# Kernel tuning notes

Measured on AMD Instinct MI355X. Metric: run time of the kernel, lower is better.

Reference implementation:

```python
import jax, jax.numpy as jnp
import numpy as np

B = 16384
D_VIS, D_LANG, D_STATE = 768, 768, 64
D = 256          # d_model
E = 4            # n_experts
K = 2            # top_k
D_IN = D_VIS + D_LANG + D_STATE
EPS = 1e-5


def layernorm(x, g, b):
    mu = x.mean(-1, keepdims=True)
    var = ((x - mu) ** 2).mean(-1, keepdims=True)
    return g * (x - mu) / jnp.sqrt(var + EPS) + b


def setup_inputs() -> dict:
    key = jax.random.key(0)
    ks = jax.random.split(key, 16)
    s = 0.02
    return {
        "vis": jax.random.normal(ks[0], (B, D_VIS), jnp.float32),
        "lang": jax.random.normal(ks[1], (B, D_LANG), jnp.float32),
        "state": jax.random.normal(ks[2], (B, D_STATE), jnp.float32),
        # fusion: Linear(d_in, d_model) + LayerNorm
        "Wf": jax.random.normal(ks[3], (D_IN, D), jnp.float32) * s,
        "bf": jnp.zeros((D,), jnp.float32),
        "gf": jnp.ones((D,), jnp.float32),
        "bfln": jnp.zeros((D,), jnp.float32),
        # gate (bias=False); random instead of zeros so routing is nontrivial
        "Wg": jax.random.normal(ks[4], (D, E), jnp.float32) * s,
        # stacked experts: Linear(d,2d) -> GELU -> Linear(2d,d) -> GELU -> Linear(d,d), then LN(x + net(x))
        "W1": jax.random.normal(ks[5], (E, D, 2 * D), jnp.float32) * s,
        "b1": jnp.zeros((E, 2 * D), jnp.float32),
        "W2": jax.random.normal(ks[6], (E, 2 * D, D), jnp.float32) * s,
        "b2": jnp.zeros((E, D), jnp.float32),
        "W3": jax.random.normal(ks[7], (E, D, D), jnp.float32) * s,
        "b3": jnp.zeros((E, D), jnp.float32),
        "eg": jnp.ones((E, D), jnp.float32),
        "eb": jnp.zeros((E, D), jnp.float32),
    }


def reference(vis, lang, state, Wf, bf, gf, bfln, Wg, W1, b1, W2, b2, W3, b3, eg, eb):
    gelu = lambda t: jax.nn.gelu(t, approximate=False)
    # fusion: Linear -> LayerNorm -> GELU  (dropout is eval-mode identity)
    x = jnp.concatenate([vis, lang, state], axis=-1) @ Wf + bf   # [B, D]
    x = gelu(layernorm(x, gf, bfln))

    logits = x @ Wg                                              # [B, E]
    all_probs = jax.nn.softmax(logits, axis=-1)
    top_vals, top_idx = jax.lax.top_k(logits, K)                 # [B, K]
    top_w = jax.nn.softmax(top_vals, axis=-1)                    # [B, K]

    # all experts densely (E small); original computes same math per masked subset
    h = gelu(jnp.einsum('bd,edh->beh', x, W1) + b1)              # [B, E, 2D]
    h = gelu(jnp.einsum('beh,ehd->bed', h, W2) + b2)             # [B, E, D]
    h = jnp.einsum('bed,edf->bef', h, W3) + b3                   # [B, E, D]
    y = layernorm(x[:, None, :] + h, eg, eb)                     # [B, E, D]

    # gather selected experts and combine with top-k weights
    y_sel = jnp.take_along_axis(y, top_idx[:, :, None], axis=1)  # [B, K, D]
    out = jnp.einsum('bk,bkd->bd', top_w, y_sel)                 # [B, D]

    # load-balance loss: importance x load
    counts = jnp.zeros((E,), x.dtype).at[top_idx.reshape(-1)].add(1.0)
    f_i = counts / (B * K)
    lb_loss = E * jnp.sum(f_i * all_probs.mean(0))
    return out, lb_loss
```

## Files before the change

### kernel.cpp

```cpp
#include <hip/hip_runtime.h>
#include <math.h>


typedef unsigned short u16;
typedef unsigned int u32;
typedef __attribute__((ext_vector_type(8))) short bf16x8;
typedef __attribute__((ext_vector_type(4))) float f32x4;

__device__ __forceinline__ float bf2f(u16 u) {
    union { u32 i; float f; } v; v.i = ((u32)u) << 16; return v.f;
}
__device__ __forceinline__ u16 f2bf(float f) {
    union { float f; u32 i; } v; v.f = f;
    u32 x = v.i;
    return (u16)((x + 0x7fffu + ((x >> 16) & 1u)) >> 16);
}
__device__ __forceinline__ float gelu_exact(float v) {
    return 0.5f * v * (1.0f + erff(v * 0.70710678118654752f));
}

typedef __attribute__((address_space(1))) void GV;
typedef __attribute__((address_space(3))) void SV;
__device__ __forceinline__ void gldlds(const void* g, void* l) {
    __builtin_amdgcn_global_load_lds((GV*)g, (SV*)l, 16, 0, 0);
}

__device__ __forceinline__ u32 pk2(u32 f0, u32 f1) {
    return __builtin_amdgcn_perm(f1, f0, 0x07060302);
}

__device__ __forceinline__ void stageA64(const u16* Ag, int lda, u16* As, int tid) {
#pragma unroll
    for (int i = 0; i < 2; ++i) {
        int s = i * 256 + tid;
        int m = s >> 3, c = s & 7;
        gldlds(Ag + m * lda + (c ^ (m & 7)) * 8, As + s * 8);
    }
}
__device__ __forceinline__ void stageA64_R32(const u16* Ag, int lda, u16* As, int tid) {
    int s = tid;
    int m = s >> 3, c = s & 7;
    gldlds(Ag + m * lda + (c ^ (m & 7)) * 8, As + s * 8);
}
__device__ __forceinline__ void stageB64(const u16* Bg, int ldb, u16* Bs, int tid) {
#pragma unroll
    for (int i = 0; i < 8; ++i) {
        int s = i * 256 + tid;
        int n = s >> 3, c = s & 7;
        gldlds(Bg + n * ldb + (c ^ (n & 7)) * 8, Bs + s * 8);
    }
}
__device__ __forceinline__ void compute64(const u16* As, const u16* Bs, f32x4 acc[4][4],
                                          int w, int l16, int quad) {
#pragma unroll
    for (int ks = 0; ks < 2; ++ks) {
        bf16x8 a[4];
#pragma unroll
        for (int mt = 0; mt < 4; ++mt) {
            int m = mt * 16 + l16;
            a[mt] = *(const bf16x8*)(As + m * 64 + (((ks * 4 + quad) ^ (m & 7)) << 3));
        }
#pragma unroll
        for (int nt = 0; nt < 4; ++nt) {
            int n = w * 64 + nt * 16 + l16;
            bf16x8 b = *(const bf16x8*)(Bs + n * 64 + (((ks * 4 + quad) ^ (n & 7)) << 3));
#pragma unroll
            for (int mt = 0; mt < 4; ++mt)
                acc[mt][nt] = __builtin_amdgcn_mfma_f32_16x16x32_bf16(a[mt], b, acc[mt][nt], 0, 0, 0);
        }
    }
}
__device__ __forceinline__ void compute64_R32(const u16* As, const u16* Bs, f32x4 acc[2][4],
                                              int w, int l16, int quad) {
#pragma unroll
    for (int ks = 0; ks < 2; ++ks) {
        bf16x8 a[2];
#pragma unroll
        for (int mt = 0; mt < 2; ++mt) {
            int m = mt * 16 + l16;
            a[mt] = *(const bf16x8*)(As + m * 64 + (((ks * 4 + quad) ^ (m & 7)) << 3));
        }
#pragma unroll
        for (int nt = 0; nt < 4; ++nt) {
            int n = w * 64 + nt * 16 + l16;
            bf16x8 b = *(const bf16x8*)(Bs + n * 64 + (((ks * 4 + quad) ^ (n & 7)) << 3));
#pragma unroll
            for (int mt = 0; mt < 2; ++mt)
                acc[mt][nt] = __builtin_amdgcn_mfma_f32_16x16x32_bf16(a[mt], b, acc[mt][nt], 0, 0, 0);
        }
    }
}

#define SEG_WF  409600
#define SEG_W1  524288
#define SEG_W2  524288
#define SEG_W3  262144
#define PREP_ITEMS (SEG_WF + SEG_W1 + SEG_W2 + SEG_W3 + 8)

__global__ __launch_bounds__(256) void prep_kernel(
    const float* __restrict__ Wf, const float* __restrict__ W1, const float* __restrict__ W2,
    const float* __restrict__ W3,
    u16* __restrict__ wft, u16* __restrict__ w1t, u16* __restrict__ w2t, u16* __restrict__ w3t,
    float* __restrict__ lbacc) {
    int idx = blockIdx.x * 256 + threadIdx.x;
    if (idx < SEG_WF) {
        int n = idx / 1600, k = idx % 1600;
        wft[idx] = f2bf(Wf[(size_t)k * 256 + n]);
        return;
    }
    idx -= SEG_WF;
    if (idx < SEG_W1) {
        int e = idx >> 17, r = idx & 131071;
        int n = r >> 8, k = r & 255;
        w1t[idx] = f2bf(W1[(size_t)e * 131072 + (size_t)k * 512 + n]);
        return;
    }
    idx -= SEG_W1;
    if (idx < SEG_W2) {
        int e = idx >> 17, r = idx & 131071;
        int n = r >> 9, k = r & 511;
        w2t[idx] = f2bf(W2[(size_t)e * 131072 + (size_t)k * 256 + n]);
        return;
    }
    idx -= SEG_W2;
    if (idx < SEG_W3) {
        int e = idx >> 16, r = idx & 65535;
        int n = r >> 8, k = r & 255;
        w3t[idx] = f2bf(W3[(size_t)e * 65536 + (size_t)k * 256 + n]);
        return;
    }
    idx -= SEG_W3;
    if (idx < 8) lbacc[idx] = 0.0f;
}

__global__ __launch_bounds__(256) void fusion_kernel(
    const float* __restrict__ vis, const float* __restrict__ lang, const float* __restrict__ state,
    const u16* __restrict__ BT, const float* __restrict__ bfv_, const float* __restrict__ gf,
    const float* __restrict__ bfln, const float* __restrict__ Wg,
    u16* __restrict__ xbf, float* __restrict__ wr, float* __restrict__ lbacc) {
    __shared__ __align__(16) u32 Af[2048];
    __shared__ __align__(16) u16 Bs[16384];
    int tid = threadIdx.x;
    int w = tid >> 6, lane = tid & 63, quad = lane >> 4, l16 = lane & 15;
    int m0 = blockIdx.x * 32;
    f32x4 acc[2][4] = {};

    for (int kit = 0; kit < 25; ++kit) {
        const float* base; int ld;
        if (kit < 12)      { base = vis   + (size_t)m0 * 768 + kit * 64;        ld = 768; }
        else if (kit < 24) { base = lang  + (size_t)m0 * 768 + (kit - 12) * 64; ld = 768; }
        else               { base = state + (size_t)m0 * 64;                    ld = 64; }
#pragma unroll
        for (int i = 0; i < 2; ++i) {
            int s = i * 256 + tid;
            int m = s >> 4, c = s & 15;
            gldlds(base + m * ld + (c ^ (m & 15)) * 4, Af + s * 4);
        }
        stageB64(BT + kit * 64, 1600, Bs, tid);
        __syncthreads();
#pragma unroll
        for (int ks = 0; ks < 2; ++ks) {
            bf16x8 a[2];
#pragma unroll
            for (int mt = 0; mt < 2; ++mt) {
                int m = mt * 16 + l16;
                int c0 = ks * 8 + quad * 2;
                const u32* rowp = Af + m * 64;
                uint4 f0 = *(const uint4*)(rowp + (c0 ^ (m & 15)) * 4);
                uint4 f1 = *(const uint4*)(rowp + ((c0 + 1) ^ (m & 15)) * 4);
                union { u32 u[4]; bf16x8 v; } pk;
                pk.u[0] = pk2(f0.x, f0.y); pk.u[1] = pk2(f0.z, f0.w);
                pk.u[2] = pk2(f1.x, f1.y); pk.u[3] = pk2(f1.z, f1.w);
                a[mt] = pk.v;
            }
#pragma unroll
            for (int nt = 0; nt < 4; ++nt) {
                int n = w * 64 + nt * 16 + l16;
                bf16x8 b = *(const bf16x8*)(Bs + n * 64 + (((ks * 4 + quad) ^ (n & 7)) << 3));
#pragma unroll
                for (int mt = 0; mt < 2; ++mt)
                    acc[mt][nt] = __builtin_amdgcn_mfma_f32_16x16x32_bf16(a[mt], b, acc[mt][nt], 0, 0, 0);
            }
        }
        __syncthreads();
    }

    float2* red  = (float2*)Af;
    float*  muv  = (float*)(Af + 256);
    float*  rsv  = (float*)(Af + 288);
    float*  gred = (float*)(Af + 512);
    float*  sacc = (float*)(Af + 1024);

    float bv[4], gvv[4], blv[4]; float4 wgv[4];
#pragma unroll
    for (int nt = 0; nt < 4; ++nt) {
        int col = w * 64 + nt * 16 + l16;
        bv[nt] = bfv_[col]; gvv[nt] = gf[col]; blv[nt] = bfln[col];
        wgv[nt] = *(const float4*)(Wg + col * 4);
    }
    if (tid < 8) sacc[tid] = 0.f;
#pragma unroll
    for (int mt = 0; mt < 2; ++mt)
#pragma unroll
        for (int r = 0; r < 4; ++r) {
            float ss = 0.f, qq = 0.f;
#pragma unroll
            for (int nt = 0; nt < 4; ++nt) {
                float v = acc[mt][nt][r] + bv[nt];
                acc[mt][nt][r] = v;
                ss += v; qq += v * v;
            }
#pragma unroll
            for (int d = 1; d < 16; d <<= 1) { ss += __shfl_xor(ss, d); qq += __shfl_xor(qq, d); }
            if (l16 == 0) red[w * 32 + mt * 16 + quad * 4 + r] = make_float2(ss, qq);
        }
    __syncthreads();
    if (tid < 32) {
        float ss = 0.f, qq = 0.f;
#pragma unroll
        for (int ww = 0; ww < 4; ++ww) { float2 t = red[ww * 32 + tid]; ss += t.x; qq += t.y; }
        float mu = ss * (1.f / 256.f);
        float var = qq * (1.f / 256.f) - mu * mu;
        muv[tid] = mu;
        rsv[tid] = 1.f / sqrtf(var + 1e-5f);
    }
    __syncthreads();
#pragma unroll
    for (int mt = 0; mt < 2; ++mt)
#pragma unroll
        for (int r = 0; r < 4; ++r) {
            int rl = mt * 16 + quad * 4 + r;
            float mu = muv[rl], rs = rsv[rl];
#pragma unroll
            for (int nt = 0; nt < 4; ++nt) {
                int col = w * 64 + nt * 16 + l16;
                float t = (acc[mt][nt][r] - mu) * rs * gvv[nt] + blv[nt];
                float g = gelu_exact(t);
                acc[mt][nt][r] = g;
                xbf[(size_t)(m0 + rl) * 256 + col] = f2bf(g);
            }
        }
#pragma unroll
    for (int mt = 0; mt < 2; ++mt)
#pragma unroll
        for (int r = 0; r < 4; ++r) {
            int rl = mt * 16 + quad * 4 + r;
            float p0 = 0.f, p1 = 0.f, p2 = 0.f, p3 = 0.f;
#pragma unroll
            for (int nt = 0; nt < 4; ++nt) {
                float g = acc[mt][nt][r];
                p0 += g * wgv[nt].x; p1 += g * wgv[nt].y;
                p2 += g * wgv[nt].z; p3 += g * wgv[nt].w;
            }
#pragma unroll
            for (int d = 1; d < 16; d <<= 1) {
                p0 += __shfl_xor(p0, d); p1 += __shfl_xor(p1, d);
                p2 += __shfl_xor(p2, d); p3 += __shfl_xor(p3, d);
            }
            if (l16 == 0) {
                float* gp = gred + w * 128 + rl * 4;
                gp[0] = p0; gp[1] = p1; gp[2] = p2; gp[3] = p3;
            }
        }
    __syncthreads();
    if (tid < 32) {
        int row = tid;
        float lg[4];
#pragma unroll
        for (int e = 0; e < 4; ++e)
            lg[e] = gred[row * 4 + e] + gred[128 + row * 4 + e] +
                    gred[256 + row * 4 + e] + gred[384 + row * 4 + e];
        float mx = fmaxf(fmaxf(lg[0], lg[1]), fmaxf(lg[2], lg[3]));
        float ex[4]; float Z = 0.f;
#pragma unroll
        for (int e = 0; e < 4; ++e) { ex[e] = expf(lg[e] - mx); Z += ex[e]; }
        int i0 = 0; float v0 = lg[0];
#pragma unroll
        for (int e = 1; e < 4; ++e) if (lg[e] > v0) { v0 = lg[e]; i0 = e; }
        int i1 = -1; float v1 = -1e30f;
#pragma unroll
        for (int e = 0; e < 4; ++e) if (e != i0 && lg[e] > v1) { v1 = lg[e]; i1 = e; }
        float t = expf(v1 - v0);
        float wA = 1.f / (1.f + t), wB = t / (1.f + t);
        float w4[4] = {0.f, 0.f, 0.f, 0.f};
        w4[i0] = wA; w4[i1] = wB;
#pragma unroll
        for (int e = 0; e < 4; ++e) wr[(size_t)(m0 + row) * 4 + e] = w4[e];
#pragma unroll
        for (int e = 0; e < 4; ++e) atomicAdd(&sacc[e], ex[e] / Z);
        atomicAdd(&sacc[4 + i0], 1.f);
        atomicAdd(&sacc[4 + i1], 1.f);
    }
    __syncthreads();
    if (tid < 8) atomicAdd(lbacc + tid, sacc[tid]);
}

__global__ __launch_bounds__(256) void expert_gemm_kernel(
    const u16* __restrict__ A, int lda, size_t aE,
    const u16* __restrict__ BT, size_t bE,
    const float* __restrict__ bias, int biasE,
    u16* __restrict__ outp, int ldo, size_t oE) {
    __shared__ __align__(16) u16 As[4096];
    __shared__ __align__(16) u16 Bs[16384];
    int tid = threadIdx.x;
    int w = tid >> 6, lane = tid & 63, quad = lane >> 4, l16 = lane & 15;
    int m0 = blockIdx.x * 64;
    int col0 = blockIdx.y * 256;
    int e = blockIdx.z;
    f32x4 acc[4][4] = {};
    const u16* Ag = A + e * aE + (size_t)m0 * lda;
    const u16* Bg = BT + e * bE + (size_t)col0 * lda;
    int kiters = lda >> 6;
    for (int kit = 0; kit < kiters; ++kit) {
        stageA64(Ag + kit * 64, lda, As, tid);
        stageB64(Bg + kit * 64, lda, Bs, tid);
        __syncthreads();
        compute64(As, Bs, acc, w, l16, quad);
        __syncthreads();
    }
#pragma unroll
    for (int nt = 0; nt < 4; ++nt) {
        int col = col0 + w * 64 + nt * 16 + l16;
        float bvv = bias[e * biasE + col];
#pragma unroll
        for (int mt = 0; mt < 4; ++mt)
#pragma unroll
            for (int r = 0; r < 4; ++r) {
                int row = m0 + mt * 16 + quad * 4 + r;
                outp[e * oE + (size_t)row * ldo + col] = f2bf(gelu_exact(acc[mt][nt][r] + bvv));
            }
    }
}

__global__ __launch_bounds__(256) void combine_kernel(
    const u16* __restrict__ h2, const u16* __restrict__ W3T,
    const float* __restrict__ b3, const float* __restrict__ eg, const float* __restrict__ eb,
    const u16* __restrict__ xbf, const float* __restrict__ wr,
    const float* __restrict__ lbacc, float* __restrict__ outp) {
    __shared__ __align__(16) u16 As[2048];
    __shared__ __align__(16) u16 Bs[16384];
    __shared__ __align__(16) u16 xs[8192];
    __shared__ float wl[128];
    int tid = threadIdx.x;
    int w = tid >> 6, lane = tid & 63, quad = lane >> 4, l16 = lane & 15;
    int m0 = blockIdx.x * 32;
    if (blockIdx.x == 0 && tid == 0) {
        float lb = 0.f;
#pragma unroll
        for (int e = 0; e < 4; ++e)
            lb += (lbacc[4 + e] / 32768.f) * (lbacc[e] / 16384.f);
        outp[4194304] = 4.f * lb;
    }
#pragma unroll
    for (int i = 0; i < 4; ++i) {
        int s = i * 256 + tid;
        *(uint4*)(xs + s * 8) = *(const uint4*)(xbf + (size_t)m0 * 256 + s * 8);
    }
    if (tid < 128) wl[tid] = wr[(size_t)m0 * 4 + tid];
    float2* red = (float2*)As;
    float* muv = (float*)((char*)As + 1024);
    float* rsv = (float*)((char*)As + 1152);
    f32x4 oacc[2][4] = {};
    for (int e = 0; e < 4; ++e) {
        __syncthreads();
        f32x4 acc[2][4] = {};
        const u16* Ag = h2 + ((size_t)e * 16384 + m0) * 256;
        const u16* Bg = W3T + (size_t)e * 65536;
        for (int kit = 0; kit < 4; ++kit) {
            stageA64_R32(Ag + kit * 64, 256, As, tid);
            stageB64(Bg + kit * 64, 256, Bs, tid);
            __syncthreads();
            compute64_R32(As, Bs, acc, w, l16, quad);
            __syncthreads();
        }
        float b3v[4], egv[4], ebv[4];
#pragma unroll
        for (int nt = 0; nt < 4; ++nt) {
            int col = w * 64 + nt * 16 + l16;
            b3v[nt] = b3[e * 256 + col]; egv[nt] = eg[e * 256 + col]; ebv[nt] = eb[e * 256 + col];
        }
#pragma unroll
        for (int mt = 0; mt < 2; ++mt)
#pragma unroll
            for (int r = 0; r < 4; ++r) {
                int rl = mt * 16 + quad * 4 + r;
                float ss = 0.f, qq = 0.f;
#pragma unroll
                for (int nt = 0; nt < 4; ++nt) {
                    int col = w * 64 + nt * 16 + l16;
                    float v = acc[mt][nt][r] + b3v[nt] + bf2f(xs[rl * 256 + col]);
                    acc[mt][nt][r] = v;
                    ss += v; qq += v * v;
                }
#pragma unroll
                for (int d = 1; d < 16; d <<= 1) { ss += __shfl_xor(ss, d); qq += __shfl_xor(qq, d); }
                if (l16 == 0) red[w * 32 + rl] = make_float2(ss, qq);
            }
        __syncthreads();
        if (tid < 32) {
            float ss = 0.f, qq = 0.f;
#pragma unroll
            for (int ww = 0; ww < 4; ++ww) { float2 t = red[ww * 32 + tid]; ss += t.x; qq += t.y; }
            float mu = ss * (1.f / 256.f);
            float var = qq * (1.f / 256.f) - mu * mu;
            muv[tid] = mu;
            rsv[tid] = 1.f / sqrtf(var + 1e-5f);
        }
        __syncthreads();
#pragma unroll
        for (int mt = 0; mt < 2; ++mt)
#pragma unroll
            for (int r = 0; r < 4; ++r) {
                int rl = mt * 16 + quad * 4 + r;
                float mu = muv[rl], rs = rsv[rl], we = wl[rl * 4 + e];
#pragma unroll
                for (int nt = 0; nt < 4; ++nt) {
                    float y = (acc[mt][nt][r] - mu) * rs * egv[nt] + ebv[nt];
                    oacc[mt][nt][r] += we * y;
                }
            }
    }
#pragma unroll
    for (int mt = 0; mt < 2; ++mt)
#pragma unroll
        for (int r = 0; r < 4; ++r) {
            int rl = mt * 16 + quad * 4 + r;
#pragma unroll
            for (int nt = 0; nt < 4; ++nt) {
                int col = w * 64 + nt * 16 + l16;
                outp[(size_t)(m0 + rl) * 256 + col] = oacc[mt][nt][r];
            }
        }
}

extern "C" void kernel_launch(void* const* d_in, const int* in_sizes, int n_in,
                              void* d_out, int out_size, void* d_ws, size_t ws_size,
                              hipStream_t stream) {
    const float* vis   = (const float*)d_in[0];
    const float* lang  = (const float*)d_in[1];
    const float* state = (const float*)d_in[2];
    const float* Wf    = (const float*)d_in[3];
    const float* bf_   = (const float*)d_in[4];
    const float* gf    = (const float*)d_in[5];
    const float* bfln  = (const float*)d_in[6];
    const float* Wg    = (const float*)d_in[7];
    const float* W1    = (const float*)d_in[8];
    const float* b1    = (const float*)d_in[9];
    const float* W2    = (const float*)d_in[10];
    const float* b2    = (const float*)d_in[11];
    const float* W3    = (const float*)d_in[12];
    const float* b3    = (const float*)d_in[13];
    const float* eg    = (const float*)d_in[14];
    const float* eb    = (const float*)d_in[15];
    float* outp = (float*)d_out;

    char* ws = (char*)d_ws;
    size_t off = 0;
    float* lbacc = (float*)(ws + off); off += 256;
    u16* WFT  = (u16*)(ws + off); off += 819200UL;
    u16* W1T  = (u16*)(ws + off); off += 1048576UL;
    u16* W2T  = (u16*)(ws + off); off += 1048576UL;
    u16* W3T  = (u16*)(ws + off); off += 524288UL;
    u16* XBF  = (u16*)(ws + off); off += 8388608UL;
    float* WR = (float*)(ws + off); off += 262144UL;
    u16* H1   = (u16*)(ws + off); off += 67108864UL;
    u16* H2   = (u16*)(ws + off); off += 33554432UL;
    if (ws_size < off) return;

    int prep_blocks = (PREP_ITEMS + 255) / 256;
    prep_kernel<<<prep_blocks, 256, 0, stream>>>(Wf, W1, W2, W3, WFT, W1T, W2T, W3T, lbacc);
    fusion_kernel<<<512, 256, 0, stream>>>(vis, lang, state, WFT, bf_, gf, bfln, Wg,
                                           XBF, WR, lbacc);
    expert_gemm_kernel<<<dim3(256, 2, 4), 256, 0, stream>>>(
        XBF, 256, 0, W1T, 131072, b1, 512, H1, 512, 8388608UL);
    expert_gemm_kernel<<<dim3(256, 1, 4), 256, 0, stream>>>(
        H1, 512, 8388608UL, W2T, 131072, b2, 256, H2, 256, 4194304UL);
    combine_kernel<<<512, 256, 0, stream>>>(H2, W3T, b3, eg, eb, XBF, WR, lbacc, outp);
}
```

Before: 322.4 us.

## Pipeline GEMM k-loops with triple-buffered LDS and register-direct A operands

```diff
diff --git a/kernel.cpp b/kernel.cpp
--- a/kernel.cpp
+++ b/kernel.cpp
@@ -24,72 +24,11 @@
 __device__ __forceinline__ void gldlds(const void* g, void* l) {
     __builtin_amdgcn_global_load_lds((GV*)g, (SV*)l, 16, 0, 0);
 }
-
 __device__ __forceinline__ u32 pk2(u32 f0, u32 f1) {
     return __builtin_amdgcn_perm(f1, f0, 0x07060302);
 }
 
-__device__ __forceinline__ void stageA64(const u16* Ag, int lda, u16* As, int tid) {
-#pragma unroll
-    for (int i = 0; i < 2; ++i) {
-        int s = i * 256 + tid;
-        int m = s >> 3, c = s & 7;
-        gldlds(Ag + m * lda + (c ^ (m & 7)) * 8, As + s * 8);
-    }
-}
-__device__ __forceinline__ void stageA64_R32(const u16* Ag, int lda, u16* As, int tid) {
-    int s = tid;
-    int m = s >> 3, c = s & 7;
-    gldlds(Ag + m * lda + (c ^ (m & 7)) * 8, As + s * 8);
-}
-__device__ __forceinline__ void stageB64(const u16* Bg, int ldb, u16* Bs, int tid) {
-#pragma unroll
-    for (int i = 0; i < 8; ++i) {
-        int s = i * 256 + tid;
-        int n = s >> 3, c = s & 7;
-        gldlds(Bg + n * ldb + (c ^ (n & 7)) * 8, Bs + s * 8);
-    }
-}
-__device__ __forceinline__ void compute64(const u16* As, const u16* Bs, f32x4 acc[4][4],
-                                          int w, int l16, int quad) {
-#pragma unroll
-    for (int ks = 0; ks < 2; ++ks) {
-        bf16x8 a[4];
-#pragma unroll
-        for (int mt = 0; mt < 4; ++mt) {
-            int m = mt * 16 + l16;
-            a[mt] = *(const bf16x8*)(As + m * 64 + (((ks * 4 + quad) ^ (m & 7)) << 3));
-        }
-#pragma unroll
-        for (int nt = 0; nt < 4; ++nt) {
-            int n = w * 64 + nt * 16 + l16;
-            bf16x8 b = *(const bf16x8*)(Bs + n * 64 + (((ks * 4 + quad) ^ (n & 7)) << 3));
-#pragma unroll
-            for (int mt = 0; mt < 4; ++mt)
-                acc[mt][nt] = __builtin_amdgcn_mfma_f32_16x16x32_bf16(a[mt], b, acc[mt][nt], 0, 0, 0);
-        }
-    }
-}
-__device__ __forceinline__ void compute64_R32(const u16* As, const u16* Bs, f32x4 acc[2][4],
-                                              int w, int l16, int quad) {
-#pragma unroll
-    for (int ks = 0; ks < 2; ++ks) {
-        bf16x8 a[2];
-#pragma unroll
-        for (int mt = 0; mt < 2; ++mt) {
-            int m = mt * 16 + l16;
-            a[mt] = *(const bf16x8*)(As + m * 64 + (((ks * 4 + quad) ^ (m & 7)) << 3));
-        }
-#pragma unroll
-        for (int nt = 0; nt < 4; ++nt) {
-            int n = w * 64 + nt * 16 + l16;
-            bf16x8 b = *(const bf16x8*)(Bs + n * 64 + (((ks * 4 + quad) ^ (n & 7)) << 3));
-#pragma unroll
-            for (int mt = 0; mt < 2; ++mt)
-                acc[mt][nt] = __builtin_amdgcn_mfma_f32_16x16x32_bf16(a[mt], b, acc[mt][nt], 0, 0, 0);
-        }
-    }
-}
+#define FWAIT() asm volatile("s_waitcnt vmcnt(8) lgkmcnt(0)\n\ts_barrier" ::: "memory")
 
 #define SEG_WF  409600
 #define SEG_W1  524288
@@ -138,58 +77,74 @@
     const u16* __restrict__ BT, const float* __restrict__ bfv_, const float* __restrict__ gf,
     const float* __restrict__ bfln, const float* __restrict__ Wg,
     u16* __restrict__ xbf, float* __restrict__ wr, float* __restrict__ lbacc) {
-    __shared__ __align__(16) u32 Af[2048];
-    __shared__ __align__(16) u16 Bs[16384];
+    __shared__ __align__(16) u16 Bs[3][8192];
     int tid = threadIdx.x;
     int w = tid >> 6, lane = tid & 63, quad = lane >> 4, l16 = lane & 15;
     int m0 = blockIdx.x * 32;
     f32x4 acc[2][4] = {};
-
-    for (int kit = 0; kit < 25; ++kit) {
+    uint4 ar[3][2][2];
+
+    auto stage = [&](int kk, int slot) {
+#pragma unroll
+        for (int i = 0; i < 4; ++i) {
+            int s = i * 256 + tid;
+            int n = s >> 2, c = s & 3;
+            gldlds(BT + (size_t)n * 1600 + kk * 32 + ((c ^ (n & 3)) << 3), &Bs[slot][s * 8]);
+        }
+    };
+    auto loadA = [&](int kk, uint4 a[2][2]) {
         const float* base; int ld;
-        if (kit < 12)      { base = vis   + (size_t)m0 * 768 + kit * 64;        ld = 768; }
-        else if (kit < 24) { base = lang  + (size_t)m0 * 768 + (kit - 12) * 64; ld = 768; }
-        else               { base = state + (size_t)m0 * 64;                    ld = 64; }
-#pragma unroll
-        for (int i = 0; i < 2; ++i) {
-            int s = i * 256 + tid;
-            int m = s >> 4, c = s & 15;
-            gldlds(base + m * ld + (c ^ (m & 15)) * 4, Af + s * 4);
-        }
-        stageB64(BT + kit * 64, 1600, Bs, tid);
-        __syncthreads();
-#pragma unroll
-        for (int ks = 0; ks < 2; ++ks) {
-            bf16x8 a[2];
-#pragma unroll
-            for (int mt = 0; mt < 2; ++mt) {
-                int m = mt * 16 + l16;
-                int c0 = ks * 8 + quad * 2;
-                const u32* rowp = Af + m * 64;
-                uint4 f0 = *(const uint4*)(rowp + (c0 ^ (m & 15)) * 4);
-                uint4 f1 = *(const uint4*)(rowp + ((c0 + 1) ^ (m & 15)) * 4);
-                union { u32 u[4]; bf16x8 v; } pk;
-                pk.u[0] = pk2(f0.x, f0.y); pk.u[1] = pk2(f0.z, f0.w);
-                pk.u[2] = pk2(f1.x, f1.y); pk.u[3] = pk2(f1.z, f1.w);
-                a[mt] = pk.v;
-            }
-#pragma unroll
-            for (int nt = 0; nt < 4; ++nt) {
-                int n = w * 64 + nt * 16 + l16;
-                bf16x8 b = *(const bf16x8*)(Bs + n * 64 + (((ks * 4 + quad) ^ (n & 7)) << 3));
-#pragma unroll
-                for (int mt = 0; mt < 2; ++mt)
-                    acc[mt][nt] = __builtin_amdgcn_mfma_f32_16x16x32_bf16(a[mt], b, acc[mt][nt], 0, 0, 0);
-            }
-        }
-        __syncthreads();
-    }
-
-    float2* red  = (float2*)Af;
-    float*  muv  = (float*)(Af + 256);
-    float*  rsv  = (float*)(Af + 288);
-    float*  gred = (float*)(Af + 512);
-    float*  sacc = (float*)(Af + 1024);
+        if (kk < 24)      { base = vis + kk * 32;          ld = 768; }
+        else if (kk < 48) { base = lang + (kk - 24) * 32;  ld = 768; }
+        else              { base = state + (kk - 48) * 32; ld = 64; }
+#pragma unroll
+        for (int mt = 0; mt < 2; ++mt) {
+            int row = m0 + mt * 16 + l16;
+            const float* p = base + (size_t)row * ld + quad * 8;
+            a[mt][0] = *(const uint4*)p;
+            a[mt][1] = *(const uint4*)(p + 4);
+        }
+    };
+    auto comp = [&](const uint4 a[2][2], int slot) {
+        bf16x8 af[2];
+#pragma unroll
+        for (int mt = 0; mt < 2; ++mt) {
+            union { u32 u[4]; bf16x8 v; } pk;
+            pk.u[0] = pk2(a[mt][0].x, a[mt][0].y); pk.u[1] = pk2(a[mt][0].z, a[mt][0].w);
+            pk.u[2] = pk2(a[mt][1].x, a[mt][1].y); pk.u[3] = pk2(a[mt][1].z, a[mt][1].w);
+            af[mt] = pk.v;
+        }
+#pragma unroll
+        for (int nt = 0; nt < 4; ++nt) {
+            int n = w * 64 + nt * 16 + l16;
+            bf16x8 b = *(const bf16x8*)(&Bs[slot][n * 32 + ((quad ^ (n & 3)) << 3)]);
+#pragma unroll
+            for (int mt = 0; mt < 2; ++mt)
+                acc[mt][nt] = __builtin_amdgcn_mfma_f32_16x16x32_bf16(af[mt], b, acc[mt][nt], 0, 0, 0);
+        }
+    };
+
+    stage(0, 0); loadA(0, ar[0]);
+    stage(1, 1); loadA(1, ar[1]);
+    for (int kb = 0; kb < 51; kb += 3) {
+#pragma unroll
+        for (int j = 0; j < 3; ++j) {
+            int k = kb + j;
+            FWAIT();
+            int kk = (k + 2 <= 49) ? (k + 2) : 49;
+            stage(kk, (j + 2) % 3);
+            loadA(kk, ar[(j + 2) % 3]);
+            if (k < 50) comp(ar[j], j);
+        }
+    }
+    __syncthreads();
+
+    u32* SC = (u32*)(&Bs[0][0]);
+    float2* red  = (float2*)SC;
+    float*  muv  = (float*)(SC + 256);
+    float*  rsv  = (float*)(SC + 288);
+    float*  gred = (float*)(SC + 512);
+    float*  sacc = (float*)(SC + 1024);
 
     float bv[4], gvv[4], blv[4]; float4 wgv[4];
 #pragma unroll
@@ -295,39 +250,76 @@
     if (tid < 8) atomicAdd(lbacc + tid, sacc[tid]);
 }
 
-__global__ __launch_bounds__(256) void expert_gemm_kernel(
-    const u16* __restrict__ A, int lda, size_t aE,
-    const u16* __restrict__ BT, size_t bE,
+template<int KR, int KITS>
+__global__ __launch_bounds__(256) void expert_kernel(
+    const u16* __restrict__ A, int lda, long aE,
+    const u16* __restrict__ BT, int ldb, long bE,
     const float* __restrict__ bias, int biasE,
-    u16* __restrict__ outp, int ldo, size_t oE) {
-    __shared__ __align__(16) u16 As[4096];
-    __shared__ __align__(16) u16 Bs[16384];
+    u16* __restrict__ outp, int ldo, long oE) {
+    __shared__ __align__(16) u16 Bs[3][8192];
     int tid = threadIdx.x;
     int w = tid >> 6, lane = tid & 63, quad = lane >> 4, l16 = lane & 15;
     int m0 = blockIdx.x * 64;
-    int col0 = blockIdx.y * 256;
+    int n0 = blockIdx.y * 256;
     int e = blockIdx.z;
+    const u16* Ag = A + (size_t)e * aE;
+    const u16* Bg = BT + (size_t)e * bE + (size_t)n0 * ldb;
     f32x4 acc[4][4] = {};
-    const u16* Ag = A + e * aE + (size_t)m0 * lda;
-    const u16* Bg = BT + e * bE + (size_t)col0 * lda;
-    int kiters = lda >> 6;
-    for (int kit = 0; kit < kiters; ++kit) {
-        stageA64(Ag + kit * 64, lda, As, tid);
-        stageB64(Bg + kit * 64, lda, Bs, tid);
-        __syncthreads();
-        compute64(As, Bs, acc, w, l16, quad);
-        __syncthreads();
-    }
+    uint4 ar[3][4];
+
+    auto stage = [&](int kk, int slot) {
+#pragma unroll
+        for (int i = 0; i < 4; ++i) {
+            int s = i * 256 + tid;
+            int n = s >> 2, c = s & 3;
+            gldlds(Bg + (size_t)n * ldb + kk * 32 + ((c ^ (n & 3)) << 3), &Bs[slot][s * 8]);
+        }
+    };
+    auto loadA = [&](int kk, uint4 a[4]) {
+#pragma unroll
+        for (int mt = 0; mt < 4; ++mt) {
+            int row = m0 + mt * 16 + l16;
+            a[mt] = *(const uint4*)(Ag + (size_t)row * lda + kk * 32 + quad * 8);
+        }
+    };
+    auto comp = [&](const uint4 a[4], int slot) {
+#pragma unroll
+        for (int nt = 0; nt < 4; ++nt) {
+            int n = w * 64 + nt * 16 + l16;
+            bf16x8 b = *(const bf16x8*)(&Bs[slot][n * 32 + ((quad ^ (n & 3)) << 3)]);
+#pragma unroll
+            for (int mt = 0; mt < 4; ++mt) {
+                union { uint4 u; bf16x8 v; } av; av.u = a[mt];
+                acc[mt][nt] = __builtin_amdgcn_mfma_f32_16x16x32_bf16(av.v, b, acc[mt][nt], 0, 0, 0);
+            }
+        }
+    };
+
+    stage(0, 0); loadA(0, ar[0]);
+    stage(1, 1); loadA(1, ar[1]);
+    for (int kb = 0; kb < KITS; kb += 3) {
+#pragma unroll
+        for (int j = 0; j < 3; ++j) {
+            int k = kb + j;
+            FWAIT();
+            int kk = (k + 2 <= KR - 1) ? (k + 2) : (KR - 1);
+            stage(kk, (j + 2) % 3);
+            loadA(kk, ar[(j + 2) % 3]);
+            if (k < KR) comp(ar[j], j);
+        }
+    }
+    __syncthreads();
+
 #pragma unroll
     for (int nt = 0; nt < 4; ++nt) {
-        int col = col0 + w * 64 + nt * 16 + l16;
+        int col = n0 + w * 64 + nt * 16 + l16;
         float bvv = bias[e * biasE + col];
 #pragma unroll
         for (int mt = 0; mt < 4; ++mt)
 #pragma unroll
             for (int r = 0; r < 4; ++r) {
                 int row = m0 + mt * 16 + quad * 4 + r;
-                outp[e * oE + (size_t)row * ldo + col] = f2bf(gelu_exact(acc[mt][nt][r] + bvv));
+                outp[(size_t)e * oE + (size_t)row * ldo + col] = f2bf(gelu_exact(acc[mt][nt][r] + bvv));
             }
     }
 }
@@ -337,10 +329,11 @@
     const float* __restrict__ b3, const float* __restrict__ eg, const float* __restrict__ eb,
     const u16* __restrict__ xbf, const float* __restrict__ wr,
     const float* __restrict__ lbacc, float* __restrict__ outp) {
-    __shared__ __align__(16) u16 As[2048];
-    __shared__ __align__(16) u16 Bs[16384];
+    __shared__ __align__(16) u16 Bs[2][8192];
     __shared__ __align__(16) u16 xs[8192];
     __shared__ float wl[128];
+    __shared__ float2 credv[128];
+    __shared__ float cmu[32], crs[32];
     int tid = threadIdx.x;
     int w = tid >> 6, lane = tid & 63, quad = lane >> 4, l16 = lane & 15;
     int m0 = blockIdx.x * 32;
@@ -357,22 +350,49 @@
         *(uint4*)(xs + s * 8) = *(const uint4*)(xbf + (size_t)m0 * 256 + s * 8);
     }
     if (tid < 128) wl[tid] = wr[(size_t)m0 * 4 + tid];
-    float2* red = (float2*)As;
-    float* muv = (float*)((char*)As + 1024);
-    float* rsv = (float*)((char*)As + 1152);
+
     f32x4 oacc[2][4] = {};
+#pragma unroll 1
     for (int e = 0; e < 4; ++e) {
-        __syncthreads();
-        f32x4 acc[2][4] = {};
         const u16* Ag = h2 + ((size_t)e * 16384 + m0) * 256;
         const u16* Bg = W3T + (size_t)e * 65536;
-        for (int kit = 0; kit < 4; ++kit) {
-            stageA64_R32(Ag + kit * 64, 256, As, tid);
-            stageB64(Bg + kit * 64, 256, Bs, tid);
+        f32x4 acc[2][4] = {};
+        uint4 ar[2][2];
+
+        auto stage = [&](int kk, int slot) {
+#pragma unroll
+            for (int i = 0; i < 4; ++i) {
+                int s = i * 256 + tid;
+                int n = s >> 2, c = s & 3;
+                gldlds(Bg + (size_t)n * 256 + kk * 32 + ((c ^ (n & 3)) << 3), &Bs[slot][s * 8]);
+            }
+        };
+        auto loadA = [&](int kk, uint4 a[2]) {
+#pragma unroll
+            for (int mt = 0; mt < 2; ++mt) {
+                int row = m0 + mt * 16 + l16;
+                a[mt] = *(const uint4*)(Ag + (size_t)row * 256 + kk * 32 + quad * 8);
+            }
+        };
+
+        stage(0, 0); loadA(0, ar[0]);
+#pragma unroll
+        for (int k = 0; k < 8; ++k) {
             __syncthreads();
-            compute64_R32(As, Bs, acc, w, l16, quad);
-            __syncthreads();
-        }
+            if (k + 1 < 8) { stage(k + 1, (k + 1) & 1); loadA(k + 1, ar[(k + 1) & 1]); }
+#pragma unroll
+            for (int nt = 0; nt < 4; ++nt) {
+                int n = w * 64 + nt * 16 + l16;
+                bf16x8 b = *(const bf16x8*)(&Bs[k & 1][n * 32 + ((quad ^ (n & 3)) << 3)]);
+#pragma unroll
+                for (int mt = 0; mt < 2; ++mt) {
+                    union { uint4 u; bf16x8 v; } av; av.u = ar[k & 1][mt];
+                    acc[mt][nt] = __builtin_amdgcn_mfma_f32_16x16x32_bf16(av.v, b, acc[mt][nt], 0, 0, 0);
+                }
+            }
+        }
+        __syncthreads();
+
         float b3v[4], egv[4], ebv[4];
 #pragma unroll
         for (int nt = 0; nt < 4; ++nt) {
@@ -394,17 +414,17 @@
                 }
 #pragma unroll
                 for (int d = 1; d < 16; d <<= 1) { ss += __shfl_xor(ss, d); qq += __shfl_xor(qq, d); }
-                if (l16 == 0) red[w * 32 + rl] = make_float2(ss, qq);
+                if (l16 == 0) credv[w * 32 + rl] = make_float2(ss, qq);
             }
         __syncthreads();
         if (tid < 32) {
             float ss = 0.f, qq = 0.f;
 #pragma unroll
-            for (int ww = 0; ww < 4; ++ww) { float2 t = red[ww * 32 + tid]; ss += t.x; qq += t.y; }
+            for (int ww = 0; ww < 4; ++ww) { float2 t = credv[ww * 32 + tid]; ss += t.x; qq += t.y; }
             float mu = ss * (1.f / 256.f);
             float var = qq * (1.f / 256.f) - mu * mu;
-            muv[tid] = mu;
-            rsv[tid] = 1.f / sqrtf(var + 1e-5f);
+            cmu[tid] = mu;
+            crs[tid] = 1.f / sqrtf(var + 1e-5f);
         }
         __syncthreads();
 #pragma unroll
@@ -412,13 +432,14 @@
 #pragma unroll
             for (int r = 0; r < 4; ++r) {
                 int rl = mt * 16 + quad * 4 + r;
-                float mu = muv[rl], rs = rsv[rl], we = wl[rl * 4 + e];
+                float mu = cmu[rl], rs = crs[rl], we = wl[rl * 4 + e];
 #pragma unroll
                 for (int nt = 0; nt < 4; ++nt) {
                     float y = (acc[mt][nt][r] - mu) * rs * egv[nt] + ebv[nt];
                     oacc[mt][nt][r] += we * y;
                 }
             }
+        __syncthreads();
     }
 #pragma unroll
     for (int mt = 0; mt < 2; ++mt)
@@ -471,9 +492,9 @@
     prep_kernel<<<prep_blocks, 256, 0, stream>>>(Wf, W1, W2, W3, WFT, W1T, W2T, W3T, lbacc);
     fusion_kernel<<<512, 256, 0, stream>>>(vis, lang, state, WFT, bf_, gf, bfln, Wg,
                                            XBF, WR, lbacc);
-    expert_gemm_kernel<<<dim3(256, 2, 4), 256, 0, stream>>>(
-        XBF, 256, 0, W1T, 131072, b1, 512, H1, 512, 8388608UL);
-    expert_gemm_kernel<<<dim3(256, 1, 4), 256, 0, stream>>>(
-        H1, 512, 8388608UL, W2T, 131072, b2, 256, H2, 256, 4194304UL);
+    expert_kernel<8, 9><<<dim3(256, 2, 4), 256, 0, stream>>>(
+        XBF, 256, 0L, W1T, 256, 131072L, b1, 512, H1, 512, 8388608L);
+    expert_kernel<16, 18><<<dim3(256, 1, 4), 256, 0, stream>>>(
+        H1, 512, 8388608L, W2T, 512, 131072L, b2, 256, H2, 256, 4194304L);
     combine_kernel<<<512, 256, 0, stream>>>(H2, W3T, b3, eg, eb, XBF, WR, lbacc, outp);
 }
```

New measurement: 432.7 us. +34.2%, slower.
